# Kernel optimization log

Measured on AMD Instinct MI355X. Metric: run time of the kernel, lower is better.

Reference implementation:

```python
import jax, jax.numpy as jnp
import numpy as np

N_SRC, N_DST, N_EDGES, C = 100000, 40000, 500000, 128


def _mlp(x, w1, b1, w2, b2, ln_g, ln_b):
    # anemoi MLP: Linear -> SiLU -> Linear -> LayerNorm (layer_norm=True default)
    h = jax.nn.silu(x @ w1 + b1)
    y = h @ w2 + b2
    mu = jnp.mean(y, axis=-1, keepdims=True)
    var = jnp.var(y, axis=-1, keepdims=True)
    return (y - mu) * jax.lax.rsqrt(var + 1e-5) * ln_g + ln_b


def setup_inputs() -> dict:
    key = jax.random.key(0)
    ks = jax.random.split(key, 12)
    x_src = jax.random.normal(ks[0], (N_SRC, C), dtype=jnp.float32)
    x_dst = jax.random.normal(ks[1], (N_DST, C), dtype=jnp.float32)
    edge_attr = jax.random.normal(ks[2], (N_EDGES, C), dtype=jnp.float32)
    src_idx = jax.random.randint(ks[3], (N_EDGES,), 0, N_SRC)
    dst_idx = jax.random.randint(ks[4], (N_EDGES,), 0, N_DST)
    edge_index = jnp.stack([src_idx, dst_idx], axis=0)
    s = 0.02
    params = {
        # conv.edge_mlp : MLP(3C -> C -> C)
        'ew1': jax.random.normal(ks[5], (3 * C, C), dtype=jnp.float32) * s,
        'eb1': jnp.zeros((C,), jnp.float32),
        'ew2': jax.random.normal(ks[6], (C, C), dtype=jnp.float32) * s,
        'eb2': jnp.zeros((C,), jnp.float32),
        'eg': jnp.ones((C,), jnp.float32),
        'ebn': jnp.zeros((C,), jnp.float32),
        # node_mlp : MLP(2C -> C -> C)
        'nw1': jax.random.normal(ks[7], (2 * C, C), dtype=jnp.float32) * s,
        'nb1': jnp.zeros((C,), jnp.float32),
        'nw2': jax.random.normal(ks[8], (C, C), dtype=jnp.float32) * s,
        'nb2': jnp.zeros((C,), jnp.float32),
        'ng': jnp.ones((C,), jnp.float32),
        'nbn': jnp.zeros((C,), jnp.float32),
    }
    return {'x_src': x_src, 'x_dst': x_dst, 'edge_attr': edge_attr,
            'edge_index': edge_index, **params}


def reference(x_src, x_dst, edge_attr, edge_index,
              ew1, eb1, ew2, eb2, eg, ebn,
              nw1, nb1, nw2, nb2, ng, nbn):
    src_idx, dst_idx = edge_index[0], edge_index[1]
    # GraphConv message: edge_mlp(cat[x_i (dst), x_j (src), edge_attr])
    msg_in = jnp.concatenate([x_dst[dst_idx], x_src[src_idx], edge_attr], axis=1)  # [E, 3C]
    edges_new = _mlp(msg_in, ew1, eb1, ew2, eb2, eg, ebn)                          # [E, C]
    # aggregate: sum over incoming edges at dst nodes
    out = jax.ops.segment_sum(edges_new, dst_idx, num_segments=N_DST)              # [N_DST, C]
    nodes_new_dst = _mlp(jnp.concatenate([x_dst, out], axis=1),
                         nw1, nb1, nw2, nb2, ng, nbn) + x_dst
    # update_src_nodes=True
    nodes_new_src = _mlp(jnp.concatenate([x_src, x_src], axis=1),
                         nw1, nb1, nw2, nb2, ng, nbn) + x_src
    return nodes_new_src, nodes_new_dst, edges_new
```

## Files before the change

### kernel.cpp

```cpp
#include <hip/hip_runtime.h>

#define CDIM 128
#define NSRC 100000
#define NDST 40000
#define NEDGE 500000

typedef short bf8_t __attribute__((ext_vector_type(8)));
typedef float f32x4 __attribute__((ext_vector_type(4)));

static __device__ __forceinline__ unsigned short f2bf(float f) {
    unsigned int u = __float_as_uint(f);
    u = (u + 0x7fffu + ((u >> 16) & 1u)) >> 16;
    return (unsigned short)u;
}

__global__ void prep_weights(const float* __restrict__ ew1, const float* __restrict__ ew2,
                             const float* __restrict__ nw1, const float* __restrict__ nw2,
                             unsigned short* __restrict__ w1t, unsigned short* __restrict__ w2t,
                             unsigned short* __restrict__ nw1t, unsigned short* __restrict__ nw1st,
                             unsigned short* __restrict__ nw2t) {
    int i = blockIdx.x * blockDim.x + threadIdx.x;
    if (i < 128 * 384) { int n = i / 384, k = i % 384; w1t[i] = f2bf(ew1[k * 128 + n]); return; }
    i -= 128 * 384;
    if (i < 128 * 128) { int n = i / 128, k = i % 128; w2t[i] = f2bf(ew2[k * 128 + n]); return; }
    i -= 128 * 128;
    if (i < 128 * 256) { int n = i / 256, k = i % 256; nw1t[i] = f2bf(nw1[k * 128 + n]); return; }
    i -= 128 * 256;
    if (i < 128 * 128) { int n = i / 128, k = i % 128; nw1st[i] = f2bf(nw1[k * 128 + n] + nw1[(k + 128) * 128 + n]); return; }
    i -= 128 * 128;
    if (i < 128 * 128) { int n = i / 128, k = i % 128; nw2t[i] = f2bf(nw2[k * 128 + n]); return; }
}

template <int NCHUNK>
__global__ __launch_bounds__(256, 2) void mlp_fused(
    const float* __restrict__ seg0, const int* __restrict__ idx0,
    const float* __restrict__ seg1, const int* __restrict__ idx1,
    const float* __restrict__ seg2,
    const unsigned short* __restrict__ W1t, const float* __restrict__ b1,
    const unsigned short* __restrict__ W2t, const float* __restrict__ b2,
    const float* __restrict__ gamma, const float* __restrict__ beta,
    float* __restrict__ out, const float* __restrict__ residual,
    float* __restrict__ agg, const int* __restrict__ aggidx, int nrows) {

    __shared__ unsigned short Abuf[128 * 136];
    __shared__ unsigned short Wbuf[128 * 136];
    __shared__ float rstats[128][2][2];

    const int tid = threadIdx.x;
    const int lane = tid & 63;
    const int wave = tid >> 6;
    const int t = lane & 15;
    const int q = lane >> 4;
    const int rw = wave >> 1;
    const int cw = wave & 1;
    const int row0 = blockIdx.x * 128;
    const int K1 = NCHUNK * 128;

    const f32x4 zero4 = {0.f, 0.f, 0.f, 0.f};
    f32x4 acc[4][4];
#pragma unroll
    for (int a = 0; a < 4; a++)
#pragma unroll
        for (int b = 0; b < 4; b++) acc[a][b] = zero4;

#pragma unroll
    for (int c = 0; c < NCHUNK; c++) {
        {
            const float* seg = (c == 0) ? seg0 : ((c == 1) ? seg1 : seg2);
            const int* idx = (c == 0) ? idx0 : ((c == 1) ? idx1 : (const int*)nullptr);
            int r = tid >> 1;
            int hh = tid & 1;
            int grow = row0 + r;
            const float4* src = nullptr;
            if (grow < nrows) {
                long g = idx ? (long)idx[grow] : (long)grow;
                src = (const float4*)(seg + g * CDIM) + hh * 16;
            }
            unsigned short* dst = &Abuf[r * 136 + hh * 64];
#pragma unroll
            for (int i = 0; i < 16; i++) {
                float4 v = src ? src[i] : make_float4(0.f, 0.f, 0.f, 0.f);
                ushort4 p;
                p.x = f2bf(v.x); p.y = f2bf(v.y); p.z = f2bf(v.z); p.w = f2bf(v.w);
                *(ushort4*)(dst + i * 4) = p;
            }
        }
        {
            int n = tid >> 1;
            int hh = tid & 1;
            const unsigned short* src = W1t + n * K1 + c * 128 + hh * 64;
            unsigned short* dst = &Wbuf[n * 136 + hh * 64];
#pragma unroll
            for (int i = 0; i < 8; i++)
                *(int4*)(dst + i * 8) = *(const int4*)(src + i * 8);
        }
        __syncthreads();
#pragma unroll
        for (int ks = 0; ks < 4; ks++) {
            bf8_t av[4], bv[4];
#pragma unroll
            for (int mt = 0; mt < 4; mt++)
                av[mt] = *(const bf8_t*)&Abuf[(rw * 64 + mt * 16 + t) * 136 + ks * 32 + q * 8];
#pragma unroll
            for (int nt = 0; nt < 4; nt++)
                bv[nt] = *(const bf8_t*)&Wbuf[(cw * 64 + nt * 16 + t) * 136 + ks * 32 + q * 8];
#pragma unroll
            for (int mt = 0; mt < 4; mt++)
#pragma unroll
                for (int nt = 0; nt < 4; nt++)
                    acc[mt][nt] = __builtin_amdgcn_mfma_f32_16x16x32_bf16(av[mt], bv[nt], acc[mt][nt], 0, 0, 0);
        }
        __syncthreads();
    }

    unsigned short* hbuf = Abuf;
#pragma unroll
    for (int nt = 0; nt < 4; nt++) {
        int col = cw * 64 + nt * 16 + t;
        float bb = b1[col];
#pragma unroll
        for (int mt = 0; mt < 4; mt++)
#pragma unroll
            for (int r = 0; r < 4; r++) {
                float v = acc[mt][nt][r] + bb;
                v = v / (1.f + __expf(-v));
                hbuf[(rw * 64 + mt * 16 + q * 4 + r) * 136 + col] = f2bf(v);
            }
    }
    {
        int n = tid >> 1;
        int hh = tid & 1;
        const unsigned short* src = W2t + n * 128 + hh * 64;
        unsigned short* dst = &Wbuf[n * 136 + hh * 64];
#pragma unroll
        for (int i = 0; i < 8; i++)
            *(int4*)(dst + i * 8) = *(const int4*)(src + i * 8);
    }
    __syncthreads();

    f32x4 acc2[4][4];
#pragma unroll
    for (int a = 0; a < 4; a++)
#pragma unroll
        for (int b = 0; b < 4; b++) acc2[a][b] = zero4;
#pragma unroll
    for (int ks = 0; ks < 4; ks++) {
        bf8_t av[4], bv[4];
#pragma unroll
        for (int mt = 0; mt < 4; mt++)
            av[mt] = *(const bf8_t*)&hbuf[(rw * 64 + mt * 16 + t) * 136 + ks * 32 + q * 8];
#pragma unroll
        for (int nt = 0; nt < 4; nt++)
            bv[nt] = *(const bf8_t*)&Wbuf[(cw * 64 + nt * 16 + t) * 136 + ks * 32 + q * 8];
#pragma unroll
        for (int mt = 0; mt < 4; mt++)
#pragma unroll
            for (int nt = 0; nt < 4; nt++)
                acc2[mt][nt] = __builtin_amdgcn_mfma_f32_16x16x32_bf16(av[mt], bv[nt], acc2[mt][nt], 0, 0, 0);
    }

#pragma unroll
    for (int nt = 0; nt < 4; nt++) {
        float bb = b2[cw * 64 + nt * 16 + t];
#pragma unroll
        for (int mt = 0; mt < 4; mt++)
#pragma unroll
            for (int r = 0; r < 4; r++) acc2[mt][nt][r] += bb;
    }
#pragma unroll
    for (int mt = 0; mt < 4; mt++)
#pragma unroll
        for (int r = 0; r < 4; r++) {
            float s = 0.f, s2 = 0.f;
#pragma unroll
            for (int nt = 0; nt < 4; nt++) {
                float v = acc2[mt][nt][r];
                s += v; s2 += v * v;
            }
#pragma unroll
            for (int m = 1; m < 16; m <<= 1) {
                s += __shfl_xor(s, m);
                s2 += __shfl_xor(s2, m);
            }
            if (t == 0) {
                int rr = rw * 64 + mt * 16 + q * 4 + r;
                rstats[rr][cw][0] = s;
                rstats[rr][cw][1] = s2;
            }
        }
    __syncthreads();

    float gam[4], bet[4];
#pragma unroll
    for (int nt = 0; nt < 4; nt++) {
        int col = cw * 64 + nt * 16 + t;
        gam[nt] = gamma[col];
        bet[nt] = beta[col];
    }
#pragma unroll
    for (int mt = 0; mt < 4; mt++)
#pragma unroll
        for (int r = 0; r < 4; r++) {
            int rr = rw * 64 + mt * 16 + q * 4 + r;
            float s = rstats[rr][0][0] + rstats[rr][1][0];
            float s2 = rstats[rr][0][1] + rstats[rr][1][1];
            float mu = s * (1.f / 128.f);
            float var = s2 * (1.f / 128.f) - mu * mu;
            float rs = rsqrtf(var + 1e-5f);
            int grow = row0 + rr;
            if (grow < nrows) {
                int gi = agg ? aggidx[grow] : 0;
#pragma unroll
                for (int nt = 0; nt < 4; nt++) {
                    int col = cw * 64 + nt * 16 + t;
                    float o = (acc2[mt][nt][r] - mu) * rs * gam[nt] + bet[nt];
                    if (residual) o += residual[(long)grow * CDIM + col];
                    out[(long)grow * CDIM + col] = o;
                    if (agg) unsafeAtomicAdd(&agg[(long)gi * CDIM + col], o);
                }
            }
        }
}

extern "C" void kernel_launch(void* const* d_in, const int* in_sizes, int n_in,
                              void* d_out, int out_size, void* d_ws, size_t ws_size,
                              hipStream_t stream) {
    const float* x_src = (const float*)d_in[0];
    const float* x_dst = (const float*)d_in[1];
    const float* edge_attr = (const float*)d_in[2];
    const int* edge_index = (const int*)d_in[3];
    const float* ew1 = (const float*)d_in[4];
    const float* eb1 = (const float*)d_in[5];
    const float* ew2 = (const float*)d_in[6];
    const float* eb2 = (const float*)d_in[7];
    const float* eg = (const float*)d_in[8];
    const float* ebn = (const float*)d_in[9];
    const float* nw1 = (const float*)d_in[10];
    const float* nb1 = (const float*)d_in[11];
    const float* nw2 = (const float*)d_in[12];
    const float* nb2 = (const float*)d_in[13];
    const float* ng = (const float*)d_in[14];
    const float* nbn = (const float*)d_in[15];

    const int* src_idx = edge_index;
    const int* dst_idx = edge_index + NEDGE;

    float* out_src = (float*)d_out;
    float* out_dst = out_src + (size_t)NSRC * CDIM;
    float* out_edge = out_dst + (size_t)NDST * CDIM;

    char* ws = (char*)d_ws;
    float* agg = (float*)ws;
    size_t off = (size_t)NDST * CDIM * sizeof(float);
    unsigned short* w1t = (unsigned short*)(ws + off);  off += (size_t)128 * 384 * 2;
    unsigned short* w2t = (unsigned short*)(ws + off);  off += (size_t)128 * 128 * 2;
    unsigned short* nw1t = (unsigned short*)(ws + off); off += (size_t)128 * 256 * 2;
    unsigned short* nw1st = (unsigned short*)(ws + off); off += (size_t)128 * 128 * 2;
    unsigned short* nw2t = (unsigned short*)(ws + off); off += (size_t)128 * 128 * 2;

    hipMemsetAsync(agg, 0, (size_t)NDST * CDIM * sizeof(float), stream);
    prep_weights<<<(131072 + 255) / 256, 256, 0, stream>>>(ew1, ew2, nw1, nw2, w1t, w2t, nw1t, nw1st, nw2t);

    mlp_fused<3><<<(NEDGE + 127) / 128, 256, 0, stream>>>(
        x_dst, dst_idx, x_src, src_idx, edge_attr,
        w1t, eb1, w2t, eb2, eg, ebn,
        out_edge, nullptr, agg, dst_idx, NEDGE);

    mlp_fused<2><<<(NDST + 127) / 128, 256, 0, stream>>>(
        x_dst, nullptr, agg, nullptr, nullptr,
        nw1t, nb1, nw2t, nb2, ng, nbn,
        out_dst, x_dst, nullptr, nullptr, NDST);

    mlp_fused<1><<<(NSRC + 127) / 128, 256, 0, stream>>>(
        x_src, nullptr, nullptr, nullptr, nullptr,
        nw1st, nb1, nw2t, nb2, ng, nbn,
        out_src, x_src, nullptr, nullptr, NSRC);
}
```

Before: 1.016 ms.

## Pre-cast node features to bf16 and read weights directly from global memory

Adds a prep pass that casts x_src and x_dst to bf16 in the workspace, so the edge MLP's gathers of source and destination rows move half the bytes. The weight tiles are no longer staged through shared memory; each wave loads its B fragments straight from global or L2. Dropping the LDS weight buffer allows launch bounds of 4 blocks per CU instead of 2. The risks are extra cast passes over the node arrays, more repeated global traffic for weights, and a fallback path that depends on the workspace size.

Result: slower. 1.074 ms (+5.7%).

```diff
diff --git a/kernel.cpp b/kernel.cpp
--- a/kernel.cpp
+++ b/kernel.cpp
@@ -7,6 +7,7 @@
 
 typedef short bf8_t __attribute__((ext_vector_type(8)));
 typedef float f32x4 __attribute__((ext_vector_type(4)));
+typedef unsigned short u16x8 __attribute__((ext_vector_type(8)));
 
 static __device__ __forceinline__ unsigned short f2bf(float f) {
     unsigned int u = __float_as_uint(f);
@@ -31,11 +32,21 @@
     if (i < 128 * 128) { int n = i / 128, k = i % 128; nw2t[i] = f2bf(nw2[k * 128 + n]); return; }
 }
 
-template <int NCHUNK>
-__global__ __launch_bounds__(256, 2) void mlp_fused(
-    const float* __restrict__ seg0, const int* __restrict__ idx0,
-    const float* __restrict__ seg1, const int* __restrict__ idx1,
-    const float* __restrict__ seg2,
+__global__ void prep_cast(const float* __restrict__ src, unsigned short* __restrict__ dst, long n) {
+    long i = ((long)blockIdx.x * blockDim.x + threadIdx.x) * 8;
+    if (i >= n) return;
+    float4 a = *(const float4*)(src + i);
+    float4 b = *(const float4*)(src + i + 4);
+    u16x8 p = {f2bf(a.x), f2bf(a.y), f2bf(a.z), f2bf(a.w),
+               f2bf(b.x), f2bf(b.y), f2bf(b.z), f2bf(b.w)};
+    *(u16x8*)(dst + i) = p;
+}
+
+template <int NCHUNK, int BFMASK>
+__global__ __launch_bounds__(256, 4) void mlp_fused(
+    const void* __restrict__ seg0, const int* __restrict__ idx0,
+    const void* __restrict__ seg1, const int* __restrict__ idx1,
+    const void* __restrict__ seg2,
     const unsigned short* __restrict__ W1t, const float* __restrict__ b1,
     const unsigned short* __restrict__ W2t, const float* __restrict__ b2,
     const float* __restrict__ gamma, const float* __restrict__ beta,
@@ -43,7 +54,6 @@
     float* __restrict__ agg, const int* __restrict__ aggidx, int nrows) {
 
     __shared__ unsigned short Abuf[128 * 136];
-    __shared__ unsigned short Wbuf[128 * 136];
     __shared__ float rstats[128][2][2];
 
     const int tid = threadIdx.x;
@@ -56,6 +66,9 @@
     const int row0 = blockIdx.x * 128;
     const int K1 = NCHUNK * 128;
 
+    const unsigned short* W1base = W1t + (size_t)(cw * 64 + t) * K1;
+    const unsigned short* W2base = W2t + (size_t)(cw * 64 + t) * 128;
+
     const f32x4 zero4 = {0.f, 0.f, 0.f, 0.f};
     f32x4 acc[4][4];
 #pragma unroll
@@ -66,44 +79,46 @@
 #pragma unroll
     for (int c = 0; c < NCHUNK; c++) {
         {
-            const float* seg = (c == 0) ? seg0 : ((c == 1) ? seg1 : seg2);
+            const void* seg = (c == 0) ? seg0 : ((c == 1) ? seg1 : seg2);
             const int* idx = (c == 0) ? idx0 : ((c == 1) ? idx1 : (const int*)nullptr);
+            const bool isbf = ((BFMASK >> c) & 1) != 0;
             int r = tid >> 1;
             int hh = tid & 1;
             int grow = row0 + r;
-            const float4* src = nullptr;
-            if (grow < nrows) {
-                long g = idx ? (long)idx[grow] : (long)grow;
-                src = (const float4*)(seg + g * CDIM) + hh * 16;
-            }
+            bool valid = grow < nrows;
+            long g = valid ? (idx ? (long)idx[grow] : (long)grow) : 0;
             unsigned short* dst = &Abuf[r * 136 + hh * 64];
-#pragma unroll
-            for (int i = 0; i < 16; i++) {
-                float4 v = src ? src[i] : make_float4(0.f, 0.f, 0.f, 0.f);
-                ushort4 p;
-                p.x = f2bf(v.x); p.y = f2bf(v.y); p.z = f2bf(v.z); p.w = f2bf(v.w);
-                *(ushort4*)(dst + i * 4) = p;
-            }
-        }
-        {
-            int n = tid >> 1;
-            int hh = tid & 1;
-            const unsigned short* src = W1t + n * K1 + c * 128 + hh * 64;
-            unsigned short* dst = &Wbuf[n * 136 + hh * 64];
-#pragma unroll
-            for (int i = 0; i < 8; i++)
-                *(int4*)(dst + i * 8) = *(const int4*)(src + i * 8);
+            if (isbf) {
+                const int4* s = (const int4*)((const unsigned short*)seg + g * CDIM + hh * 64);
+                const int4 z4 = {0, 0, 0, 0};
+#pragma unroll
+                for (int i = 0; i < 8; i++) {
+                    int4 v = valid ? s[i] : z4;
+                    *(int4*)(dst + i * 8) = v;
+                }
+            } else {
+                const float4* s = (const float4*)((const float*)seg + g * CDIM + hh * 64);
+                const float4 f40 = make_float4(0.f, 0.f, 0.f, 0.f);
+#pragma unroll
+                for (int i = 0; i < 8; i++) {
+                    float4 va = valid ? s[2 * i] : f40;
+                    float4 vb = valid ? s[2 * i + 1] : f40;
+                    u16x8 p = {f2bf(va.x), f2bf(va.y), f2bf(va.z), f2bf(va.w),
+                               f2bf(vb.x), f2bf(vb.y), f2bf(vb.z), f2bf(vb.w)};
+                    *(u16x8*)(dst + i * 8) = p;
+                }
+            }
         }
         __syncthreads();
 #pragma unroll
         for (int ks = 0; ks < 4; ks++) {
             bf8_t av[4], bv[4];
 #pragma unroll
+            for (int nt = 0; nt < 4; nt++)
+                bv[nt] = *(const bf8_t*)(W1base + (size_t)(nt * 16) * K1 + c * 128 + ks * 32 + q * 8);
+#pragma unroll
             for (int mt = 0; mt < 4; mt++)
                 av[mt] = *(const bf8_t*)&Abuf[(rw * 64 + mt * 16 + t) * 136 + ks * 32 + q * 8];
-#pragma unroll
-            for (int nt = 0; nt < 4; nt++)
-                bv[nt] = *(const bf8_t*)&Wbuf[(cw * 64 + nt * 16 + t) * 136 + ks * 32 + q * 8];
 #pragma unroll
             for (int mt = 0; mt < 4; mt++)
 #pragma unroll
@@ -127,15 +142,6 @@
                 hbuf[(rw * 64 + mt * 16 + q * 4 + r) * 136 + col] = f2bf(v);
             }
     }
-    {
-        int n = tid >> 1;
-        int hh = tid & 1;
-        const unsigned short* src = W2t + n * 128 + hh * 64;
-        unsigned short* dst = &Wbuf[n * 136 + hh * 64];
-#pragma unroll
-        for (int i = 0; i < 8; i++)
-            *(int4*)(dst + i * 8) = *(const int4*)(src + i * 8);
-    }
     __syncthreads();
 
     f32x4 acc2[4][4];
@@ -147,11 +153,11 @@
     for (int ks = 0; ks < 4; ks++) {
         bf8_t av[4], bv[4];
 #pragma unroll
+        for (int nt = 0; nt < 4; nt++)
+            bv[nt] = *(const bf8_t*)(W2base + (size_t)(nt * 16) * 128 + ks * 32 + q * 8);
+#pragma unroll
         for (int mt = 0; mt < 4; mt++)
             av[mt] = *(const bf8_t*)&hbuf[(rw * 64 + mt * 16 + t) * 136 + ks * 32 + q * 8];
-#pragma unroll
-        for (int nt = 0; nt < 4; nt++)
-            bv[nt] = *(const bf8_t*)&Wbuf[(cw * 64 + nt * 16 + t) * 136 + ks * 32 + q * 8];
 #pragma unroll
         for (int mt = 0; mt < 4; mt++)
 #pragma unroll
@@ -252,27 +258,50 @@
     char* ws = (char*)d_ws;
     float* agg = (float*)ws;
     size_t off = (size_t)NDST * CDIM * sizeof(float);
-    unsigned short* w1t = (unsigned short*)(ws + off);  off += (size_t)128 * 384 * 2;
-    unsigned short* w2t = (unsigned short*)(ws + off);  off += (size_t)128 * 128 * 2;
-    unsigned short* nw1t = (unsigned short*)(ws + off); off += (size_t)128 * 256 * 2;
+    unsigned short* w1t = (unsigned short*)(ws + off);   off += (size_t)128 * 384 * 2;
+    unsigned short* w2t = (unsigned short*)(ws + off);   off += (size_t)128 * 128 * 2;
+    unsigned short* nw1t = (unsigned short*)(ws + off);  off += (size_t)128 * 256 * 2;
     unsigned short* nw1st = (unsigned short*)(ws + off); off += (size_t)128 * 128 * 2;
-    unsigned short* nw2t = (unsigned short*)(ws + off); off += (size_t)128 * 128 * 2;
+    unsigned short* nw2t = (unsigned short*)(ws + off);  off += (size_t)128 * 128 * 2;
+    unsigned short* xsrc_bf = (unsigned short*)(ws + off); off += (size_t)NSRC * CDIM * 2;
+    unsigned short* xdst_bf = (unsigned short*)(ws + off); off += (size_t)NDST * CDIM * 2;
+    const bool use_bf = (ws_size >= off);
 
     hipMemsetAsync(agg, 0, (size_t)NDST * CDIM * sizeof(float), stream);
-    prep_weights<<<(131072 + 255) / 256, 256, 0, stream>>>(ew1, ew2, nw1, nw2, w1t, w2t, nw1t, nw1st, nw2t);
-
-    mlp_fused<3><<<(NEDGE + 127) / 128, 256, 0, stream>>>(
-        x_dst, dst_idx, x_src, src_idx, edge_attr,
-        w1t, eb1, w2t, eb2, eg, ebn,
-        out_edge, nullptr, agg, dst_idx, NEDGE);
-
-    mlp_fused<2><<<(NDST + 127) / 128, 256, 0, stream>>>(
-        x_dst, nullptr, agg, nullptr, nullptr,
-        nw1t, nb1, nw2t, nb2, ng, nbn,
-        out_dst, x_dst, nullptr, nullptr, NDST);
-
-    mlp_fused<1><<<(NSRC + 127) / 128, 256, 0, stream>>>(
-        x_src, nullptr, nullptr, nullptr, nullptr,
-        nw1st, nb1, nw2t, nb2, ng, nbn,
-        out_src, x_src, nullptr, nullptr, NSRC);
-}
+    prep_weights<<<131072 / 256, 256, 0, stream>>>(ew1, ew2, nw1, nw2, w1t, w2t, nw1t, nw1st, nw2t);
+
+    if (use_bf) {
+        prep_cast<<<(NSRC * CDIM / 8 + 255) / 256, 256, 0, stream>>>(x_src, xsrc_bf, (long)NSRC * CDIM);
+        prep_cast<<<(NDST * CDIM / 8 + 255) / 256, 256, 0, stream>>>(x_dst, xdst_bf, (long)NDST * CDIM);
+
+        mlp_fused<3, 0b011><<<(NEDGE + 127) / 128, 256, 0, stream>>>(
+            xdst_bf, dst_idx, xsrc_bf, src_idx, edge_attr,
+            w1t, eb1, w2t, eb2, eg, ebn,
+            out_edge, nullptr, agg, dst_idx, NEDGE);
+
+        mlp_fused<2, 0b01><<<(NDST + 127) / 128, 256, 0, stream>>>(
+            xdst_bf, nullptr, agg, nullptr, nullptr,
+            nw1t, nb1, nw2t, nb2, ng, nbn,
+            out_dst, x_dst, nullptr, nullptr, NDST);
+
+        mlp_fused<1, 0b1><<<(NSRC + 127) / 128, 256, 0, stream>>>(
+            xsrc_bf, nullptr, nullptr, nullptr, nullptr,
+            nw1st, nb1, nw2t, nb2, ng, nbn,
+            out_src, x_src, nullptr, nullptr, NSRC);
+    } else {
+        mlp_fused<3, 0><<<(NEDGE + 127) / 128, 256, 0, stream>>>(
+            x_dst, dst_idx, x_src, src_idx, edge_attr,
+            w1t, eb1, w2t, eb2, eg, ebn,
+            out_edge, nullptr, agg, dst_idx, NEDGE);
+
+        mlp_fused<2, 0><<<(NDST + 127) / 128, 256, 0, stream>>>(
+            x_dst, nullptr, agg, nullptr, nullptr,
+            nw1t, nb1, nw2t, nb2, ng, nbn,
+            out_dst, x_dst, nullptr, nullptr, NDST);
+
+        mlp_fused<1, 0><<<(NSRC + 127) / 128, 256, 0, stream>>>(
+            x_src, nullptr, nullptr, nullptr, nullptr,
+            nw1st, nb1, nw2t, nb2, ng, nbn,
+            out_src, x_src, nullptr, nullptr, NSRC);
+    }
+}
```
